# Kernel optimization log

Hardware: AMD Instinct MI355X
Metric: run time of the kernel (lower is better)

## Reference

```python
import jax, jax.numpy as jnp
import numpy as np

N = 50000          # nodes
E = 800000         # edges (avg degree 16)
C = 64             # hidden_channels
MC = 128           # message_channels = 2*C
EDGE_IN = 3 * C + 4
UPD_IN = C + MC + C


def _mlp(x, w1, b1, w2, b2, w3, b3):
    h1 = jax.nn.gelu(x @ w1 + b1, approximate=False)  # torch nn.GELU default = exact erf
    h2 = jax.nn.gelu(h1 @ w2 + b2, approximate=False)
    return h2 @ w3 + b3


def _layernorm(x, g, b, eps=1e-5):
    mu = x.mean(-1, keepdims=True)
    var = ((x - mu) ** 2).mean(-1, keepdims=True)
    return (x - mu) * jax.lax.rsqrt(var + eps) * g + b


def _forward(edge_index, coords, h, flow_dir, ln_g, ln_b,
             ew1, eb1, ew2, eb2, ew3, eb3,
             gw1, gb1, gw2, gb2,
             glw1, glb1, glw2, glb2, glw3, glb3,
             uw1, ub1, uw2, ub2, uw3, ub3, res_scale):
    x = coords[0]                       # [N,3]
    feat = _layernorm(h[0], ln_g, ln_b) # [N,C]
    u = flow_dir[0]
    u = u / (jnp.linalg.norm(u) + 1e-8)
    row, col = edge_index[0], edge_index[1]
    xi, xj = x[row], x[col]             # [E,3] gathers
    rel = xi - xj
    dist2 = (rel * rel).sum(-1, keepdims=True)
    xi_dot_u = (xi * u).sum(-1, keepdims=True)
    xj_dot_u = (xj * u).sum(-1, keepdims=True)
    rel_dot_u = (rel * u).sum(-1, keepdims=True)
    fi, fj = feat[row], feat[col]       # [E,C]
    fd = fi - fj
    edge_input = jnp.concatenate([fi, fj, fd, dist2, xi_dot_u, xj_dot_u, rel_dot_u], axis=-1)  # [E, 3C+4]
    edge_hidden = _mlp(edge_input, ew1, eb1, ew2, eb2, ew3, eb3)  # [E, MC]
    gate = jax.nn.sigmoid(jax.nn.gelu(edge_hidden @ gw1 + gb1, approximate=False) @ gw2 + gb2)  # [E,1]
    msg = gate * edge_hidden
    agg = jax.ops.segment_sum(msg, row, num_segments=N)                       # [N, MC]
    deg = jax.ops.segment_sum(jnp.ones((E, 1), feat.dtype), row, num_segments=N)
    agg = agg / jnp.maximum(deg, 1.0)
    global_feat = feat.mean(0, keepdims=True)                                  # [1,C]
    global_ctx = _mlp(global_feat, glw1, glb1, glw2, glb2, glw3, glb3)        # [1,C]
    global_node = jnp.broadcast_to(global_ctx, (feat.shape[0], global_ctx.shape[-1]))
    update_input = jnp.concatenate([feat, agg, global_node], axis=-1)          # [N, C+MC+C]
    dh = _mlp(update_input, uw1, ub1, uw2, ub2, uw3, ub3)                      # [N,C]
    return (jnp.tanh(res_scale) * dh)[None]                                    # [1,N,C]


def setup_inputs() -> dict:
    key = jax.random.key(0)
    ks = iter(jax.random.split(key, 40))
    def nrm(shape, scale=0.05):
        return (jax.random.normal(next(ks), shape, jnp.float32) * scale)
    return {
        "coords": jax.random.normal(next(ks), (1, N, 3), jnp.float32),
        "h": jax.random.normal(next(ks), (1, N, C), jnp.float32),
        "flow_dir": jax.random.normal(next(ks), (1, 3), jnp.float32),
        "edge_index": jax.random.randint(next(ks), (2, E), 0, N, dtype=jnp.int32),
        "ln_g": jnp.ones((C,), jnp.float32), "ln_b": jnp.zeros((C,), jnp.float32),
        "ew1": nrm((EDGE_IN, MC)), "eb1": jnp.zeros((MC,), jnp.float32),
        "ew2": nrm((MC, MC)), "eb2": jnp.zeros((MC,), jnp.float32),
        "ew3": nrm((MC, MC)), "eb3": jnp.zeros((MC,), jnp.float32),
        "gw1": nrm((MC, MC)), "gb1": jnp.zeros((MC,), jnp.float32),
        "gw2": nrm((MC, 1)), "gb2": jnp.zeros((1,), jnp.float32),
        "glw1": nrm((C, C)), "glb1": jnp.zeros((C,), jnp.float32),
        "glw2": nrm((C, C)), "glb2": jnp.zeros((C,), jnp.float32),
        "glw3": nrm((C, C)), "glb3": jnp.zeros((C,), jnp.float32),
        "uw1": nrm((UPD_IN, MC)), "ub1": jnp.zeros((MC,), jnp.float32),
        "uw2": nrm((MC, MC)), "ub2": jnp.zeros((MC,), jnp.float32),
        "uw3": nrm((MC, C)), "ub3": jnp.zeros((C,), jnp.float32),
        "res_scale": jnp.float32(0.15),
    }


def reference(coords, h, flow_dir, edge_index, ln_g, ln_b,
              ew1, eb1, ew2, eb2, ew3, eb3,
              gw1, gb1, gw2, gb2,
              glw1, glb1, glw2, glb2, glw3, glb3,
              uw1, ub1, uw2, ub2, uw3, ub3, res_scale):
    return _forward(edge_index, coords, h, flow_dir, ln_g, ln_b,
                    ew1, eb1, ew2, eb2, ew3, eb3,
                    gw1, gb1, gw2, gb2,
                    glw1, glb1, glw2, glb2, glw3, glb3,
                    uw1, ub1, uw2, ub2, uw3, ub3, res_scale)
```

## Files before the change

kernel.cpp:

```cpp
#include <hip/hip_runtime.h>
#include <hip/hip_bf16.h>
#include <math.h>

#define N_NODES 50000
#define N_EDGES 800000
#define CDIM 64
#define MCDIM 128
#define GSUM_REP 32

#define XS1 168
#define HS  136
#define UST 264

typedef __attribute__((ext_vector_type(8))) short short8;
typedef __attribute__((ext_vector_type(4))) float floatx4;
typedef __attribute__((ext_vector_type(2))) float f32x2;

__device__ __forceinline__ float gelu_fast(float x) {
    float z = fabsf(x) * 0.70710678f;
    float w = fmaf(z, fmaf(z, fmaf(z, fmaf(z, 0.078108f, 0.000972f),
                                   0.230389f), 0.278393f), 1.0f);
    float w2 = w * w;
    float r = __builtin_amdgcn_rcpf(w2 * w2);
    float m = 0.5f * fabsf(x);
    return fmaf(-m, r, fmaf(0.5f, x, m));
}

__device__ __forceinline__ f32x2 gelu_pk(f32x2 x) {
    f32x2 ax = __builtin_elementwise_abs(x);
    f32x2 z = ax * 0.70710678f;
    f32x2 w = z * (z * (z * (z * 0.078108f + 0.000972f) + 0.230389f)
                   + 0.278393f) + 1.0f;
    f32x2 w2 = w * w;
    f32x2 w4 = w2 * w2;
    f32x2 r;
    r.x = __builtin_amdgcn_rcpf(w4.x);
    r.y = __builtin_amdgcn_rcpf(w4.y);
    f32x2 m = 0.5f * ax;
    return 0.5f * x + m - m * r;
}

__device__ __forceinline__ unsigned short f2bf(float f) {
    unsigned int u = __float_as_uint(f);
    unsigned int r = u + 0x7fffu + ((u >> 16) & 1u);
    return (unsigned short)(r >> 16);
}
__device__ __forceinline__ float bf2f(unsigned int lo16) {
    return __uint_as_float(lo16 << 16);
}
__device__ __forceinline__ unsigned int f2bf2(float lo, float hi) {
    __hip_bfloat162 v = __float22bfloat162_rn(make_float2(lo, hi));
    union { __hip_bfloat162 b; unsigned int u; } cv;
    cv.b = v;
    return cv.u;
}
__device__ __forceinline__ ushort4 pack4(float4 v) {
    ushort4 r;
    r.x = f2bf(v.x); r.y = f2bf(v.y); r.z = f2bf(v.z); r.w = f2bf(v.w);
    return r;
}

#define F1_OFF 0
#define F2_OFF (5 * 4096)
#define F3_OFF (9 * 4096)
#define FG_OFF (13 * 4096)
#define FU1_OFF (17 * 4096)
#define FU2_OFF (25 * 4096)
#define FU3_OFF (29 * 4096)
#define FRAG_TOTAL (29 * 4096 + 4 * 2048)

__global__ __launch_bounds__(256) void prep_frags(
    const float* __restrict__ ew1, const float* __restrict__ ew2,
    const float* __restrict__ ew3, const float* __restrict__ gw1,
    const float* __restrict__ eb3, const float* __restrict__ gb1,
    const float* __restrict__ uw1, const float* __restrict__ uw2,
    const float* __restrict__ uw3, unsigned short* __restrict__ frags,
    int* __restrict__ deg_int, float* __restrict__ gsum,
    float* __restrict__ egb) {
    int idx = blockIdx.x * 256 + threadIdx.x;
    if (idx < N_NODES) deg_int[idx] = 0;
    if (idx < GSUM_REP * 64) gsum[idx] = 0.0f;
    if (idx < 128) {
        float s = gb1[idx];
        for (int jj = 0; jj < 128; jj++) s += eb3[jj] * gw1[jj * 128 + idx];
        egb[idx] = s;
    }
    if (idx >= FRAG_TOTAL) return;
    if (idx < F2_OFF) {
        int chunk = idx >> 12;
        int rem = idx & 4095;
        int ct = rem >> 9;
        int lane = (rem >> 3) & 63;
        int j = rem & 7;
        int k = chunk * 32 + (lane >> 4) * 8 + j;
        int n = ct * 16 + (lane & 15);
        float v;
        if (k < 64)       v = ew1[k * 128 + n] + ew1[(128 + k) * 128 + n];
        else if (k < 128) v = ew1[k * 128 + n] - ew1[(64 + k) * 128 + n];
        else if (k < 132) v = ew1[(192 + k - 128) * 128 + n];
        else              v = 0.0f;
        frags[idx] = f2bf(v);
    } else if (idx >= FG_OFF && idx < FU1_OFF) {
        int chunk = idx >> 12;
        int rem = idx & 4095;
        int ct = rem >> 9;
        int lane = (rem >> 3) & 63;
        int j = rem & 7;
        int k = (chunk - 13) * 32 + (lane >> 4) * 8 + j;
        int n = ct * 16 + (lane & 15);
        float s = 0.0f;
        for (int jj = 0; jj < 128; jj++) s += ew3[k * 128 + jj] * gw1[jj * 128 + n];
        frags[idx] = f2bf(s);
    } else if (idx < FU3_OFF) {
        int chunk = idx >> 12;
        int rem = idx & 4095;
        int ct = rem >> 9;
        int lane = (rem >> 3) & 63;
        int j = rem & 7;
        const float* W; int kbase;
        if (chunk < 9)       { W = ew2; kbase = (chunk - 5) * 32; }
        else if (chunk < 13) { W = ew3; kbase = (chunk - 9) * 32; }
        else if (chunk < 25) { W = uw1; kbase = (chunk - 17) * 32; }
        else                 { W = uw2; kbase = (chunk - 25) * 32; }
        int k = kbase + (lane >> 4) * 8 + j;
        int n = ct * 16 + (lane & 15);
        frags[idx] = f2bf(W[k * 128 + n]);
    } else {
        int rem = idx - FU3_OFF;
        int chunk = rem >> 11;
        int r = rem & 2047;
        int ct = r >> 9;
        int lane = (r >> 3) & 63;
        int j = r & 7;
        int k = chunk * 32 + (lane >> 4) * 8 + j;
        int n = ct * 16 + (lane & 15);
        frags[idx] = f2bf(uw3[k * 64 + n]);
    }
}

template <int NCT>
__device__ __forceinline__ void bias_init(floatx4* acc,
                                          const float* __restrict__ bias, int lane) {
    int c = lane & 15;
#pragma unroll
    for (int ct = 0; ct < NCT; ct++) {
        float b = bias[ct * 16 + c];
        acc[ct][0] = b; acc[ct][1] = b; acc[ct][2] = b; acc[ct][3] = b;
    }
}

template <int NCH, int NCT>
__device__ __forceinline__ void mfma_layer(const unsigned short* Xl, int xs,
                                           const unsigned short* __restrict__ F,
                                           int lane, floatx4* acc) {
    int q = lane >> 4, c = lane & 15;
    const unsigned short* xrow = Xl + c * xs + q * 8;
    for (int k0 = 0; k0 < NCH; k0++) {
        short8 a = *(const short8*)(xrow + k0 * 32);
#pragma unroll
        for (int ct = 0; ct < NCT; ct++) {
            short8 b = *(const short8*)(F + ((k0 * NCT + ct) * 64 + lane) * 8);
            acc[ct] = __builtin_amdgcn_mfma_f32_16x16x32_bf16(a, b, acc[ct], 0, 0, 0);
        }
    }
}

template <int NCH>
__device__ __forceinline__ void mfma_nsplit(const unsigned short* x1, int rstride,
                                            const unsigned short* __restrict__ F,
                                            int lane, int w2,
                                            floatx4 acc[4][2]) {
    int q = lane >> 4, c = lane & 15;
    for (int k0 = 0; k0 < NCH; k0++) {
        short8 b0 = *(const short8*)(F + (((k0 * 8 + w2) * 64) + lane) * 8);
        short8 b1 = *(const short8*)(F + (((k0 * 8 + w2 + 1) * 64) + lane) * 8);
#pragma unroll
        for (int rt = 0; rt < 4; rt++) {
            short8 a = *(const short8*)(x1 + rt * (16 * XS1) + c * rstride
                                        + q * 8 + k0 * 32);
            acc[rt][0] = __builtin_amdgcn_mfma_f32_16x16x32_bf16(a, b0, acc[rt][0], 0, 0, 0);
            acc[rt][1] = __builtin_amdgcn_mfma_f32_16x16x32_bf16(a, b1, acc[rt][1], 0, 0, 0);
        }
    }
}

__device__ __forceinline__ void bias_init2(floatx4 acc[4][2],
                                           const float* __restrict__ bias,
                                           int lane, int w) {
    int c = lane & 15;
    float b0 = bias[w * 32 + c], b1 = bias[w * 32 + 16 + c];
#pragma unroll
    for (int rt = 0; rt < 4; rt++) {
        acc[rt][0][0] = b0; acc[rt][0][1] = b0; acc[rt][0][2] = b0; acc[rt][0][3] = b0;
        acc[rt][1][0] = b1; acc[rt][1][1] = b1; acc[rt][1][2] = b1; acc[rt][1][3] = b1;
    }
}

__device__ __forceinline__ void epi2_store(floatx4 acc[4][2],
                                           unsigned short* x1, int lane, int w) {
    int q = lane >> 4, c = lane & 15;
#pragma unroll
    for (int rt = 0; rt < 4; rt++) {
        unsigned short* base = x1 + rt * (16 * XS1) + (q * 4) * HS + w * 32 + c;
#pragma unroll
        for (int ctl = 0; ctl < 2; ctl++) {
            f32x2 v01 = {acc[rt][ctl][0], acc[rt][ctl][1]};
            f32x2 v23 = {acc[rt][ctl][2], acc[rt][ctl][3]};
            v01 = gelu_pk(v01); v23 = gelu_pk(v23);
            unsigned int p01 = f2bf2(v01.x, v01.y), p23 = f2bf2(v23.x, v23.y);
            unsigned short* p = base + ctl * 16;
            p[0]      = (unsigned short)p01;
            p[HS]     = (unsigned short)(p01 >> 16);
            p[2 * HS] = (unsigned short)p23;
            p[3 * HS] = (unsigned short)(p23 >> 16);
        }
    }
}

template <bool GELU, int NCT>
__device__ __forceinline__ void epilogue_store(floatx4* acc,
                                               unsigned short* dst, int xs, int lane) {
    int q = lane >> 4, c = lane & 15;
    unsigned short* base = dst + (q * 4) * xs + c;
#pragma unroll
    for (int ct = 0; ct < NCT; ct++) {
        f32x2 v01 = {acc[ct][0], acc[ct][1]};
        f32x2 v23 = {acc[ct][2], acc[ct][3]};
        if (GELU) { v01 = gelu_pk(v01); v23 = gelu_pk(v23); }
        unsigned int p01 = f2bf2(v01.x, v01.y), p23 = f2bf2(v23.x, v23.y);
        unsigned short* p = base + ct * 16;
        p[0]      = (unsigned short)p01;
        p[xs]     = (unsigned short)(p01 >> 16);
        p[2 * xs] = (unsigned short)p23;
        p[3 * xs] = (unsigned short)(p23 >> 16);
    }
}

__global__ __launch_bounds__(256) void ln_count_kernel(
    const float* __restrict__ h, const float* __restrict__ ln_g,
    const float* __restrict__ ln_b, const float* __restrict__ flow_dir,
    const int* __restrict__ eidx, unsigned short* __restrict__ featb,
    float* __restrict__ gsum, float* __restrict__ u_out,
    int* __restrict__ deg_int) {
    int t = threadIdx.x;
    int ln = t >> 6;
    int c = t & 63;
    int n = blockIdx.x * 4 + ln;

    float x = h[n * CDIM + c];
    float s = x;
#pragma unroll
    for (int off = 32; off > 0; off >>= 1) s += __shfl_xor(s, off, 64);
    float mu = s * (1.0f / 64.0f);
    float d = x - mu;
    float v = d * d;
#pragma unroll
    for (int off = 32; off > 0; off >>= 1) v += __shfl_xor(v, off, 64);
    float rs = 1.0f / sqrtf(v * (1.0f / 64.0f) + 1e-5f);
    float f = d * rs * ln_g[c] + ln_b[c];
    featb[n * CDIM + c] = f2bf(f);

    __shared__ float fs[4][64];
    fs[ln][c] = f;
    __syncthreads();
    if (t < 64) {
        float p = fs[0][t] + fs[1][t] + fs[2][t] + fs[3][t];
        atomicAdd(&gsum[(blockIdx.x & (GSUM_REP - 1)) * 64 + t], p);
        int e = blockIdx.x * 64 + t;
        atomicAdd(&deg_int[eidx[e]], 1);
    }
    if (blockIdx.x == 0 && t == 0) {
        float ux = flow_dir[0], uy = flow_dir[1], uz = flow_dir[2];
        float nrm = sqrtf(ux * ux + uy * uy + uz * uz) + 1e-8f;
        u_out[0] = ux / nrm;
        u_out[1] = uy / nrm;
        u_out[2] = uz / nrm;
    }
}

__global__ __launch_bounds__(1024) void mid_kernel(
    const int* __restrict__ deg_int, int* __restrict__ rowstart,
    int* __restrict__ cursor,
    const float* __restrict__ gsum,
    const float* __restrict__ glw1, const float* __restrict__ glb1,
    const float* __restrict__ glw2, const float* __restrict__ glb2,
    const float* __restrict__ glw3, const float* __restrict__ glb3,
    const float* __restrict__ res_scale,
    unsigned short* __restrict__ gctxb, float* __restrict__ tres) {
    int t = threadIdx.x;
    if (blockIdx.x == 0) {
        __shared__ int wsum[16];
        __shared__ int run;
        int wid = t >> 6, lane = t & 63;
        int4 vs[13];
#pragma unroll
        for (int chunk = 0; chunk < 13; chunk++) {
            int base = chunk * 4096 + t * 4;
            int4 v = {0, 0, 0, 0};
            if (base + 3 < N_NODES) {
                v = *(const int4*)(deg_int + base);
            } else {
                if (base < N_NODES) v.x = deg_int[base];
                if (base + 1 < N_NODES) v.y = deg_int[base + 1];
                if (base + 2 < N_NODES) v.z = deg_int[base + 2];
                if (base + 3 < N_NODES) v.w = deg_int[base + 3];
            }
            vs[chunk] = v;
        }
        if (t == 0) run = 0;
        __syncthreads();
#pragma unroll
        for (int chunk = 0; chunk < 13; chunk++) {
            int base = chunk * 4096 + t * 4;
            int4 v = vs[chunk];
            int s1 = v.x, s2 = s1 + v.y, s3 = s2 + v.z, s4 = s3 + v.w;
            int x = s4;
#pragma unroll
            for (int off = 1; off < 64; off <<= 1) {
                int y = __shfl_up(x, off, 64);
                if (lane >= off) x += y;
            }
            if (lane == 63) wsum[wid] = x;
            __syncthreads();
            if (t < 16) {
                int sv = wsum[t];
#pragma unroll
                for (int off = 1; off < 16; off <<= 1) {
                    int y = __shfl_up(sv, off, 16);
                    if (t >= off) sv += y;
                }
                wsum[t] = sv;
            }
            __syncthreads();
            int run_l = run;
            int wpre = (wid == 0) ? 0 : wsum[wid - 1];
            int toff = run_l + wpre + (x - s4);
            int e0 = toff, e1 = toff + s1, e2 = toff + s2, e3 = toff + s3;
            if (base <= N_NODES) rowstart[base] = e0;
            if (base + 1 <= N_NODES) rowstart[base + 1] = e1;
            if (base + 2 <= N_NODES) rowstart[base + 2] = e2;
            if (base + 3 <= N_NODES) rowstart[base + 3] = e3;
            if (base < N_NODES) cursor[base] = e0;
            if (base + 1 < N_NODES) cursor[base + 1] = e1;
            if (base + 2 < N_NODES) cursor[base + 2] = e2;
            if (base + 3 < N_NODES) cursor[base + 3] = e3;
            __syncthreads();
            if (t == 0) run = run_l + wsum[15];
            __syncthreads();
        }
    } else {
        __shared__ float a[64], b[64];
        float s = 0.0f;
        if (t < 64) {
            float acc = 0.0f;
            for (int r = 0; r < GSUM_REP; r++) acc += gsum[r * 64 + t];
            a[t] = acc * (1.0f / (float)N_NODES);
        }
        __syncthreads();
        if (t < 64) {
            s = glb1[t];
            for (int k = 0; k < 64; k++) s += a[k] * glw1[k * 64 + t];
            b[t] = gelu_fast(s);
        }
        __syncthreads();
        if (t < 64) {
            s = glb2[t];
            for (int k = 0; k < 64; k++) s += b[k] * glw2[k * 64 + t];
        }
        __syncthreads();
        if (t < 64) a[t] = gelu_fast(s);
        __syncthreads();
        if (t < 64) {
            s = glb3[t];
            for (int k = 0; k < 64; k++) s += a[k] * glw3[k * 64 + t];
            gctxb[t] = f2bf(s);
        }
        if (t == 0) *tres = tanhf(res_scale[0]);
    }
}

struct SmemE {
    unsigned short x1[64 * XS1];
    float gatep[4][64];
    int pos[64];
    int rows[64];
};

__global__ __launch_bounds__(256, 6) void edge_kernel(
    const float* __restrict__ coords, const int* __restrict__ eidx,
    const unsigned short* __restrict__ featb, const float* __restrict__ u,
    const unsigned short* __restrict__ frags,
    const float* __restrict__ eb1, const float* __restrict__ eb2,
    const float* __restrict__ eb3,
    const float* __restrict__ egb, const float* __restrict__ gw2,
    const float* __restrict__ gb2,
    int* __restrict__ cursor, unsigned short* __restrict__ msg,
    float* __restrict__ agg, int use_msg) {
    __shared__ SmemE sm;
    int t = threadIdx.x;
    int wv = t >> 6;
    int lane = t & 63;
    int e0 = blockIdx.x * 64;
    int q = lane >> 4, c = lane & 15;
    int w2 = wv * 2;

    int rowreg;
    {
        int le = t >> 2, sub = t & 3;
        int e = e0 + le;
        int row = eidx[e];
        int col = eidx[N_EDGES + e];
        rowreg = row;
        const uint4* fi4 = (const uint4*)(featb + (long)row * CDIM);
        const uint4* fj4 = (const uint4*)(featb + (long)col * CDIM);
        unsigned short* xr = sm.x1 + le * XS1;
        *(uint4*)(xr + sub * 16) = fi4[sub * 2];
        *(uint4*)(xr + sub * 16 + 8) = fi4[sub * 2 + 1];
        *(uint4*)(xr + 64 + sub * 16) = fj4[sub * 2];
        *(uint4*)(xr + 64 + sub * 16 + 8) = fj4[sub * 2 + 1];
        ushort4 z = {0, 0, 0, 0};
        if (sub == 0) {
            sm.rows[le] = row;
            float xix = coords[row * 3], xiy = coords[row * 3 + 1], xiz = coords[row * 3 + 2];
            float xjx = coords[col * 3], xjy = coords[col * 3 + 1], xjz = coords[col * 3 + 2];
            float rx = xix - xjx, ry = xiy - xjy, rz = xiz - xjz;
            float ux = u[0], uy = u[1], uz = u[2];
            float4 sc;
            sc.x = rx * rx + ry * ry + rz * rz;
            sc.y = xix * ux + xiy * uy + xiz * uz;
            sc.z = xjx * ux + xjy * uy + xjz * uz;
            sc.w = rx * ux + ry * uy + rz * uz;
            *(ushort4*)(xr + 128) = pack4(sc);
        } else if (sub == 1) {
            *(ushort4*)(xr + 132) = z; *(ushort4*)(xr + 136) = z; *(ushort4*)(xr + 140) = z;
        } else if (sub == 2) {
            *(ushort4*)(xr + 144) = z; *(ushort4*)(xr + 148) = z;
        } else {
            *(ushort4*)(xr + 152) = z; *(ushort4*)(xr + 156) = z;
        }
    }
    __syncthreads();

    floatx4 acc[4][2];

    bias_init2(acc, eb1, lane, wv);
    mfma_nsplit<5>(sm.x1, XS1, frags + F1_OFF, lane, w2, acc);
    __syncthreads();
    epi2_store(acc, sm.x1, lane, wv);
    __syncthreads();

    bias_init2(acc, eb2, lane, wv);
    mfma_nsplit<4>(sm.x1, HS, frags + F2_OFF, lane, w2, acc);
    __syncthreads();
    epi2_store(acc, sm.x1, lane, wv);
    __syncthreads();

    int posreg = 0;
    if (use_msg && (t & 3) == 0) posreg = atomicAdd(&cursor[rowreg], 1);

    bias_init2(acc, egb, lane, wv);
    mfma_nsplit<4>(sm.x1, HS, frags + FG_OFF, lane, w2, acc);
    {
#pragma unroll
        for (int rt = 0; rt < 4; rt++) {
            float w2v0 = gw2[wv * 32 + c];
            float w2v1 = gw2[wv * 32 + 16 + c];
            f32x2 g01a = gelu_pk((f32x2){acc[rt][0][0], acc[rt][0][1]});
            f32x2 g23a = gelu_pk((f32x2){acc[rt][0][2], acc[rt][0][3]});
            f32x2 g01b = gelu_pk((f32x2){acc[rt][1][0], acc[rt][1][1]});
            f32x2 g23b = gelu_pk((f32x2){acc[rt][1][2], acc[rt][1][3]});
            float p[4];
            p[0] = g01a.x * w2v0 + g01b.x * w2v1;
            p[1] = g01a.y * w2v0 + g01b.y * w2v1;
            p[2] = g23a.x * w2v0 + g23b.x * w2v1;
            p[3] = g23a.y * w2v0 + g23b.y * w2v1;
#pragma unroll
            for (int i = 0; i < 4; i++) {
#pragma unroll
                for (int mask = 1; mask < 16; mask <<= 1)
                    p[i] += __shfl_xor(p[i], mask, 64);
            }
            if (c == 0) {
#pragma unroll
                for (int i = 0; i < 4; i++)
                    sm.gatep[wv][rt * 16 + q * 4 + i] = p[i];
            }
        }
    }

    floatx4 acch[4][2];
    bias_init2(acch, eb3, lane, wv);
    mfma_nsplit<4>(sm.x1, HS, frags + F3_OFF, lane, w2, acch);
    __syncthreads();

    float gb = gb2[0];
    float g4[4][4];
#pragma unroll
    for (int rt = 0; rt < 4; rt++) {
#pragma unroll
        for (int i = 0; i < 4; i++) {
            int e = rt * 16 + q * 4 + i;
            float z = sm.gatep[0][e] + sm.gatep[1][e] + sm.gatep[2][e]
                    + sm.gatep[3][e] + gb;
            g4[rt][i] = 1.0f / (1.0f + __expf(-z));
        }
    }

    if (use_msg) {
        {
#pragma unroll
            for (int rt = 0; rt < 4; rt++) {
                unsigned short* base = sm.x1 + rt * (16 * XS1) + (q * 4) * HS
                                     + wv * 32 + c;
#pragma unroll
                for (int ctl = 0; ctl < 2; ctl++) {
                    unsigned int p01 = f2bf2(acch[rt][ctl][0] * g4[rt][0],
                                             acch[rt][ctl][1] * g4[rt][1]);
                    unsigned int p23 = f2bf2(acch[rt][ctl][2] * g4[rt][2],
                                             acch[rt][ctl][3] * g4[rt][3]);
                    unsigned short* p = base + ctl * 16;
                    p[0]      = (unsigned short)p01;
                    p[HS]     = (unsigned short)(p01 >> 16);
                    p[2 * HS] = (unsigned short)p23;
                    p[3 * HS] = (unsigned short)(p23 >> 16);
                }
            }
        }
        if ((t & 3) == 0) sm.pos[t >> 2] = posreg;
        __syncthreads();
        {
            int le = t >> 2, sub = t & 3;
            long base = (long)sm.pos[le] * MCDIM;
            const unsigned short* src = sm.x1 + (le >> 4) * 16 * XS1 + (le & 15) * HS;
#pragma unroll
            for (int m = 0; m < 4; m++) {
                int off = m * 32 + sub * 8;
                *(short8*)(msg + base + off) = *(const short8*)(src + off);
            }
        }
    } else {
#pragma unroll
        for (int rt = 0; rt < 4; rt++) {
#pragma unroll
            for (int i = 0; i < 4; i++) {
                int row = sm.rows[rt * 16 + q * 4 + i];
                float* agr = agg + (long)row * MCDIM + wv * 32 + c;
#pragma unroll
                for (int ctl = 0; ctl < 2; ctl++)
                    atomicAdd(agr + ctl * 16, g4[rt][i] * acch[rt][ctl][i]);
            }
        }
    }
}

__global__ __launch_bounds__(256) void gather_kernel(
    const int* __restrict__ rowstart, const unsigned short* __restrict__ msg,
    const float* __restrict__ agg, int use_msg,
    unsigned short* __restrict__ aggb) {
    int wv = threadIdx.x >> 6, lane = threadIdx.x & 63;
    int n = blockIdx.x * 4 + wv;
    if (n >= N_NODES) return;
    int rs = rowstart[n], re = rowstart[n + 1];
    int deg = re - rs;
    float a0 = 0.0f, a1 = 0.0f, a2 = 0.0f, a3 = 0.0f;
    if (use_msg) {
        const unsigned short* base = msg + (long)rs * MCDIM;
        int pairs = deg >> 1;
        for (int i = 0; i < pairs; i++) {
            uint2 v = *(const uint2*)(base + i * 256 + lane * 4);
            a0 += bf2f(v.x & 0xffffu); a1 += bf2f(v.x >> 16);
            a2 += bf2f(v.y & 0xffffu); a3 += bf2f(v.y >> 16);
        }
        if ((deg & 1) && lane < 32) {
            uint2 v = *(const uint2*)(base + (deg - 1) * MCDIM + lane * 4);
            a0 += bf2f(v.x & 0xffffu); a1 += bf2f(v.x >> 16);
            a2 += bf2f(v.y & 0xffffu); a3 += bf2f(v.y >> 16);
        }
        a0 += __shfl_xor(a0, 32, 64);
        a1 += __shfl_xor(a1, 32, 64);
        a2 += __shfl_xor(a2, 32, 64);
        a3 += __shfl_xor(a3, 32, 64);
    } else if (lane < 32) {
        const float4 v = *(const float4*)(agg + (long)n * MCDIM + lane * 4);
        a0 = v.x; a1 = v.y; a2 = v.z; a3 = v.w;
    }
    if (lane < 32) {
        float inv = 1.0f / fmaxf((float)deg, 1.0f);
        uint2 o;
        o.x = f2bf2(a0 * inv, a1 * inv);
        o.y = f2bf2(a2 * inv, a3 * inv);
        *(uint2*)(aggb + (long)n * MCDIM + lane * 4) = o;
    }
}

struct SmemU {
    unsigned short ui[64 * UST];
};

__global__ __launch_bounds__(256, 4) void update_kernel(
    const unsigned short* __restrict__ featb, const unsigned short* __restrict__ aggb,
    const unsigned short* __restrict__ gctxb, const float* __restrict__ tres,
    const unsigned short* __restrict__ frags,
    const float* __restrict__ ub1, const float* __restrict__ ub2,
    const float* __restrict__ ub3,
    float* __restrict__ out) {
    __shared__ SmemU sm;
    int t = threadIdx.x;
    int wv = t >> 6;
    int lane = t & 63;
    int n0 = blockIdx.x * 64;
    unsigned short* slice = sm.ui + wv * 16 * UST;

    {
        int ln = t >> 2, sub = t & 3;
        int n = n0 + ln;
        unsigned short* ur = sm.ui + ln * UST;
        if (n < N_NODES) {
            const uint4* f4 = (const uint4*)(featb + (long)n * CDIM);
            *(uint4*)(ur + sub * 16) = f4[sub * 2];
            *(uint4*)(ur + sub * 16 + 8) = f4[sub * 2 + 1];
            const uint4* a4 = (const uint4*)(aggb + (long)n * MCDIM);
            *(uint4*)(ur + 64 + sub * 32) = a4[sub * 4];
            *(uint4*)(ur + 64 + sub * 32 + 8) = a4[sub * 4 + 1];
            *(uint4*)(ur + 64 + sub * 32 + 16) = a4[sub * 4 + 2];
            *(uint4*)(ur + 64 + sub * 32 + 24) = a4[sub * 4 + 3];
            const uint4* g4 = (const uint4*)gctxb;
            *(uint4*)(ur + 192 + sub * 16) = g4[sub * 2];
            *(uint4*)(ur + 192 + sub * 16 + 8) = g4[sub * 2 + 1];
        } else {
            uint4 z = {0, 0, 0, 0};
#pragma unroll
            for (int m = 0; m < 8; m++) *(uint4*)(ur + sub * 64 + m * 8) = z;
        }
    }
    __syncthreads();

    floatx4 acc[8];
    bias_init<8>(acc, ub1, lane);
    mfma_layer<8, 8>(slice, UST, frags + FU1_OFF, lane, acc);
    epilogue_store<true, 8>(acc, slice, HS, lane);
    __syncthreads();

    bias_init<8>(acc, ub2, lane);
    mfma_layer<4, 8>(slice, HS, frags + FU2_OFF, lane, acc);
    epilogue_store<true, 8>(acc, slice, HS, lane);
    __syncthreads();

    floatx4 acc3[4];
    bias_init<4>(acc3, ub3, lane);
    mfma_layer<4, 4>(slice, HS, frags + FU3_OFF, lane, acc3);
    {
        int q = lane >> 4, c = lane & 15;
        float tr = *tres;
#pragma unroll
        for (int ct = 0; ct < 4; ct++) {
#pragma unroll
            for (int i = 0; i < 4; i++) {
                int n = n0 + wv * 16 + q * 4 + i;
                if (n < N_NODES) out[(long)n * CDIM + ct * 16 + c] = acc3[ct][i] * tr;
            }
        }
    }
}

extern "C" void kernel_launch(void* const* d_in, const int* in_sizes, int n_in,
                              void* d_out, int out_size, void* d_ws, size_t ws_size,
                              hipStream_t stream) {
    const float* coords = (const float*)d_in[0];
    const float* h = (const float*)d_in[1];
    const float* flow = (const float*)d_in[2];
    const int* eidx = (const int*)d_in[3];
    const float* ln_g = (const float*)d_in[4];
    const float* ln_b = (const float*)d_in[5];
    const float* ew1 = (const float*)d_in[6];
    const float* eb1 = (const float*)d_in[7];
    const float* ew2 = (const float*)d_in[8];
    const float* eb2 = (const float*)d_in[9];
    const float* ew3 = (const float*)d_in[10];
    const float* eb3 = (const float*)d_in[11];
    const float* gw1 = (const float*)d_in[12];
    const float* gb1 = (const float*)d_in[13];
    const float* gw2 = (const float*)d_in[14];
    const float* gb2 = (const float*)d_in[15];
    const float* glw1 = (const float*)d_in[16];
    const float* glb1 = (const float*)d_in[17];
    const float* glw2 = (const float*)d_in[18];
    const float* glb2 = (const float*)d_in[19];
    const float* glw3 = (const float*)d_in[20];
    const float* glb3 = (const float*)d_in[21];
    const float* uw1 = (const float*)d_in[22];
    const float* ub1 = (const float*)d_in[23];
    const float* uw2 = (const float*)d_in[24];
    const float* ub2 = (const float*)d_in[25];
    const float* uw3 = (const float*)d_in[26];
    const float* ub3 = (const float*)d_in[27];
    const float* res = (const float*)d_in[28];

    char* base = (char*)d_ws;
    unsigned short* frags = (unsigned short*)base;
    unsigned short* featb = (unsigned short*)(base + FRAG_TOTAL * 2);
    unsigned short* aggb = featb + (size_t)N_NODES * CDIM;
    unsigned short* gctxb = aggb + (size_t)N_NODES * MCDIM;
    float* gsum = (float*)(gctxb + 64);
    float* u = gsum + GSUM_REP * 64;
    float* tres = u + 4;
    float* egb = tres + 1;
    int* rowstart = (int*)(egb + 128);
    int* cursor = rowstart + (N_NODES + 1);
    int* deg_int = cursor + N_NODES;
    char* tail = (char*)(deg_int + N_NODES);
    tail = (char*)(((uintptr_t)tail + 255) & ~(uintptr_t)255);
    size_t head_bytes = (size_t)(tail - base);
    size_t msg_bytes = (size_t)N_EDGES * MCDIM * 2;
    int use_msg = (ws_size >= head_bytes + msg_bytes) ? 1 : 0;
    unsigned short* msg = (unsigned short*)tail;
    float* agg = (float*)tail;

    if (!use_msg)
        hipMemsetAsync(agg, 0, (size_t)N_NODES * MCDIM * sizeof(float), stream);

    prep_frags<<<FRAG_TOTAL / 256, 256, 0, stream>>>(ew1, ew2, ew3, gw1,
                                                     eb3, gb1,
                                                     uw1, uw2, uw3, frags,
                                                     deg_int, gsum, egb);
    ln_count_kernel<<<N_NODES / 4, 256, 0, stream>>>(h, ln_g, ln_b, flow, eidx,
                                                     featb, gsum, u, deg_int);
    mid_kernel<<<2, 1024, 0, stream>>>(deg_int, rowstart, cursor, gsum,
                                       glw1, glb1, glw2, glb2, glw3, glb3,
                                       res, gctxb, tres);
    edge_kernel<<<N_EDGES / 64, 256, 0, stream>>>(coords, eidx, featb, u, frags,
                                                  eb1, eb2, eb3, egb, gw2, gb2,
                                                  cursor, msg, agg, use_msg);
    gather_kernel<<<(N_NODES + 3) / 4, 256, 0, stream>>>(rowstart, msg, agg,
                                                         use_msg, aggb);
    update_kernel<<<(N_NODES + 63) / 64, 256, 0, stream>>>(featb, aggb, gctxb,
                                                           tres, frags,
                                                           ub1, ub2, ub3,
                                                           (float*)d_out);
}
```

Baseline: 455.9 us.

## Fuse CSR message gather into update kernel and raise edge kernel occupancy

When the message buffer path is active, the update kernel now reduces each node's CSR-sorted bf16 messages itself and writes the mean aggregate straight into shared memory. This removes the separate gather kernel launch and the round trip of the aggregated bf16 tensor through global memory. The edge kernel's launch bound also rises from 6 to 7 blocks per CU, which may force register spilling. The fused gather runs serially per wave over 16 nodes, so load imbalance and latency exposure inside the update kernel could offset the saved traffic.

```diff
diff --git a/kernel.cpp b/kernel.cpp
--- a/kernel.cpp
+++ b/kernel.cpp
@@ -386,7 +386,7 @@
     int rows[64];
 };
 
-__global__ __launch_bounds__(256, 6) void edge_kernel(
+__global__ __launch_bounds__(256, 7) void edge_kernel(
     const float* __restrict__ coords, const int* __restrict__ eidx,
     const unsigned short* __restrict__ featb, const float* __restrict__ u,
     const unsigned short* __restrict__ frags,
@@ -599,11 +599,12 @@
 
 __global__ __launch_bounds__(256, 4) void update_kernel(
     const unsigned short* __restrict__ featb, const unsigned short* __restrict__ aggb,
+    const int* __restrict__ rowstart, const unsigned short* __restrict__ msg,
     const unsigned short* __restrict__ gctxb, const float* __restrict__ tres,
     const unsigned short* __restrict__ frags,
     const float* __restrict__ ub1, const float* __restrict__ ub2,
     const float* __restrict__ ub3,
-    float* __restrict__ out) {
+    float* __restrict__ out, int use_msg) {
     __shared__ SmemU sm;
     int t = threadIdx.x;
     int wv = t >> 6;
@@ -619,11 +620,13 @@
             const uint4* f4 = (const uint4*)(featb + (long)n * CDIM);
             *(uint4*)(ur + sub * 16) = f4[sub * 2];
             *(uint4*)(ur + sub * 16 + 8) = f4[sub * 2 + 1];
-            const uint4* a4 = (const uint4*)(aggb + (long)n * MCDIM);
-            *(uint4*)(ur + 64 + sub * 32) = a4[sub * 4];
-            *(uint4*)(ur + 64 + sub * 32 + 8) = a4[sub * 4 + 1];
-            *(uint4*)(ur + 64 + sub * 32 + 16) = a4[sub * 4 + 2];
-            *(uint4*)(ur + 64 + sub * 32 + 24) = a4[sub * 4 + 3];
+            if (!use_msg) {
+                const uint4* a4 = (const uint4*)(aggb + (long)n * MCDIM);
+                *(uint4*)(ur + 64 + sub * 32) = a4[sub * 4];
+                *(uint4*)(ur + 64 + sub * 32 + 8) = a4[sub * 4 + 1];
+                *(uint4*)(ur + 64 + sub * 32 + 16) = a4[sub * 4 + 2];
+                *(uint4*)(ur + 64 + sub * 32 + 24) = a4[sub * 4 + 3];
+            }
             const uint4* g4 = (const uint4*)gctxb;
             *(uint4*)(ur + 192 + sub * 16) = g4[sub * 2];
             *(uint4*)(ur + 192 + sub * 16 + 8) = g4[sub * 2 + 1];
@@ -631,6 +634,39 @@
             uint4 z = {0, 0, 0, 0};
 #pragma unroll
             for (int m = 0; m < 8; m++) *(uint4*)(ur + sub * 64 + m * 8) = z;
+        }
+    }
+
+    if (use_msg) {
+        for (int ln2 = 0; ln2 < 16; ln2++) {
+            int n = n0 + wv * 16 + ln2;
+            if (n >= N_NODES) break;
+            int rs = rowstart[n], re = rowstart[n + 1];
+            int deg = re - rs;
+            float a0 = 0.0f, a1 = 0.0f, a2 = 0.0f, a3 = 0.0f;
+            const unsigned short* basep = msg + (long)rs * MCDIM;
+            int pairs = deg >> 1;
+            for (int i = 0; i < pairs; i++) {
+                uint2 v = *(const uint2*)(basep + i * 256 + lane * 4);
+                a0 += bf2f(v.x & 0xffffu); a1 += bf2f(v.x >> 16);
+                a2 += bf2f(v.y & 0xffffu); a3 += bf2f(v.y >> 16);
+            }
+            if ((deg & 1) && lane < 32) {
+                uint2 v = *(const uint2*)(basep + (deg - 1) * MCDIM + lane * 4);
+                a0 += bf2f(v.x & 0xffffu); a1 += bf2f(v.x >> 16);
+                a2 += bf2f(v.y & 0xffffu); a3 += bf2f(v.y >> 16);
+            }
+            a0 += __shfl_xor(a0, 32, 64);
+            a1 += __shfl_xor(a1, 32, 64);
+            a2 += __shfl_xor(a2, 32, 64);
+            a3 += __shfl_xor(a3, 32, 64);
+            if (lane < 32) {
+                float inv = 1.0f / fmaxf((float)deg, 1.0f);
+                uint2 o;
+                o.x = f2bf2(a0 * inv, a1 * inv);
+                o.y = f2bf2(a2 * inv, a3 * inv);
+                *(uint2*)(sm.ui + (wv * 16 + ln2) * UST + 64 + lane * 4) = o;
+            }
         }
     }
     __syncthreads();
@@ -731,10 +767,12 @@
     edge_kernel<<<N_EDGES / 64, 256, 0, stream>>>(coords, eidx, featb, u, frags,
                                                   eb1, eb2, eb3, egb, gw2, gb2,
                                                   cursor, msg, agg, use_msg);
-    gather_kernel<<<(N_NODES + 3) / 4, 256, 0, stream>>>(rowstart, msg, agg,
-                                                         use_msg, aggb);
-    update_kernel<<<(N_NODES + 63) / 64, 256, 0, stream>>>(featb, aggb, gctxb,
-                                                           tres, frags,
+    if (!use_msg)
+        gather_kernel<<<(N_NODES + 3) / 4, 256, 0, stream>>>(rowstart, msg, agg,
+                                                             use_msg, aggb);
+    update_kernel<<<(N_NODES + 63) / 64, 256, 0, stream>>>(featb, aggb,
+                                                           rowstart, msg,
+                                                           gctxb, tres, frags,
                                                            ub1, ub2, ub3,
-                                                           (float*)d_out);
-}
+                                                           (float*)d_out, use_msg);
+}
```

Measured after the change: 481.3 us. 5.6% more time.

## Split update MLP across output columns per wave and unroll message gather

Applied to the files above, without the earlier changes.

The update kernel switches from each wave owning 16 rows and all output columns to each wave owning all 64 rows and a slice of output columns, the same N-split scheme the edge kernel uses. This lets each weight fragment loaded from global memory be reused across four row tiles, cutting weight traffic per block, but it adds barriers between the MMA and epilogue phases because outputs now overwrite rows other waves still read. Separately, the CSR aggregation loop is unrolled by two with independent accumulators to expose more memory-level parallelism.

```diff
diff --git a/kernel.cpp b/kernel.cpp
--- a/kernel.cpp
+++ b/kernel.cpp
@@ -166,7 +166,8 @@
 }
 
 template <int NCH>
-__device__ __forceinline__ void mfma_nsplit(const unsigned short* x1, int rstride,
+__device__ __forceinline__ void mfma_nsplit(const unsigned short* x1,
+                                            int tilestride, int rstride,
                                             const unsigned short* __restrict__ F,
                                             int lane, int w2,
                                             floatx4 acc[4][2]) {
@@ -176,7 +177,7 @@
         short8 b1 = *(const short8*)(F + (((k0 * 8 + w2 + 1) * 64) + lane) * 8);
 #pragma unroll
         for (int rt = 0; rt < 4; rt++) {
-            short8 a = *(const short8*)(x1 + rt * (16 * XS1) + c * rstride
+            short8 a = *(const short8*)(x1 + rt * tilestride + c * rstride
                                         + q * 8 + k0 * 32);
             acc[rt][0] = __builtin_amdgcn_mfma_f32_16x16x32_bf16(a, b0, acc[rt][0], 0, 0, 0);
             acc[rt][1] = __builtin_amdgcn_mfma_f32_16x16x32_bf16(a, b1, acc[rt][1], 0, 0, 0);
@@ -197,11 +198,12 @@
 }
 
 __device__ __forceinline__ void epi2_store(floatx4 acc[4][2],
-                                           unsigned short* x1, int lane, int w) {
+                                           unsigned short* x1, int tilestride,
+                                           int lane, int w) {
     int q = lane >> 4, c = lane & 15;
 #pragma unroll
     for (int rt = 0; rt < 4; rt++) {
-        unsigned short* base = x1 + rt * (16 * XS1) + (q * 4) * HS + w * 32 + c;
+        unsigned short* base = x1 + rt * tilestride + (q * 4) * HS + w * 32 + c;
 #pragma unroll
         for (int ctl = 0; ctl < 2; ctl++) {
             f32x2 v01 = {acc[rt][ctl][0], acc[rt][ctl][1]};
@@ -214,25 +216,6 @@
             p[2 * HS] = (unsigned short)p23;
             p[3 * HS] = (unsigned short)(p23 >> 16);
         }
-    }
-}
-
-template <bool GELU, int NCT>
-__device__ __forceinline__ void epilogue_store(floatx4* acc,
-                                               unsigned short* dst, int xs, int lane) {
-    int q = lane >> 4, c = lane & 15;
-    unsigned short* base = dst + (q * 4) * xs + c;
-#pragma unroll
-    for (int ct = 0; ct < NCT; ct++) {
-        f32x2 v01 = {acc[ct][0], acc[ct][1]};
-        f32x2 v23 = {acc[ct][2], acc[ct][3]};
-        if (GELU) { v01 = gelu_pk(v01); v23 = gelu_pk(v23); }
-        unsigned int p01 = f2bf2(v01.x, v01.y), p23 = f2bf2(v23.x, v23.y);
-        unsigned short* p = base + ct * 16;
-        p[0]      = (unsigned short)p01;
-        p[xs]     = (unsigned short)(p01 >> 16);
-        p[2 * xs] = (unsigned short)p23;
-        p[3 * xs] = (unsigned short)(p23 >> 16);
     }
 }
 
@@ -444,22 +427,22 @@
     floatx4 acc[4][2];
 
     bias_init2(acc, eb1, lane, wv);
-    mfma_nsplit<5>(sm.x1, XS1, frags + F1_OFF, lane, w2, acc);
-    __syncthreads();
-    epi2_store(acc, sm.x1, lane, wv);
+    mfma_nsplit<5>(sm.x1, 16 * XS1, XS1, frags + F1_OFF, lane, w2, acc);
+    __syncthreads();
+    epi2_store(acc, sm.x1, 16 * XS1, lane, wv);
     __syncthreads();
 
     bias_init2(acc, eb2, lane, wv);
-    mfma_nsplit<4>(sm.x1, HS, frags + F2_OFF, lane, w2, acc);
-    __syncthreads();
-    epi2_store(acc, sm.x1, lane, wv);
+    mfma_nsplit<4>(sm.x1, 16 * XS1, HS, frags + F2_OFF, lane, w2, acc);
+    __syncthreads();
+    epi2_store(acc, sm.x1, 16 * XS1, lane, wv);
     __syncthreads();
 
     int posreg = 0;
     if (use_msg && (t & 3) == 0) posreg = atomicAdd(&cursor[rowreg], 1);
 
     bias_init2(acc, egb, lane, wv);
-    mfma_nsplit<4>(sm.x1, HS, frags + FG_OFF, lane, w2, acc);
+    mfma_nsplit<4>(sm.x1, 16 * XS1, HS, frags + FG_OFF, lane, w2, acc);
     {
 #pragma unroll
         for (int rt = 0; rt < 4; rt++) {
@@ -490,7 +473,7 @@
 
     floatx4 acch[4][2];
     bias_init2(acch, eb3, lane, wv);
-    mfma_nsplit<4>(sm.x1, HS, frags + F3_OFF, lane, w2, acch);
+    mfma_nsplit<4>(sm.x1, 16 * XS1, HS, frags + F3_OFF, lane, w2, acch);
     __syncthreads();
 
     float gb = gb2[0];
@@ -566,11 +549,22 @@
     if (use_msg) {
         const unsigned short* base = msg + (long)rs * MCDIM;
         int pairs = deg >> 1;
-        for (int i = 0; i < pairs; i++) {
+        float b0 = 0.0f, b1 = 0.0f, b2 = 0.0f, b3 = 0.0f;
+        int i = 0;
+        for (; i + 1 < pairs; i += 2) {
+            uint2 v = *(const uint2*)(base + i * 256 + lane * 4);
+            uint2 w = *(const uint2*)(base + (i + 1) * 256 + lane * 4);
+            a0 += bf2f(v.x & 0xffffu); a1 += bf2f(v.x >> 16);
+            a2 += bf2f(v.y & 0xffffu); a3 += bf2f(v.y >> 16);
+            b0 += bf2f(w.x & 0xffffu); b1 += bf2f(w.x >> 16);
+            b2 += bf2f(w.y & 0xffffu); b3 += bf2f(w.y >> 16);
+        }
+        if (i < pairs) {
             uint2 v = *(const uint2*)(base + i * 256 + lane * 4);
             a0 += bf2f(v.x & 0xffffu); a1 += bf2f(v.x >> 16);
             a2 += bf2f(v.y & 0xffffu); a3 += bf2f(v.y >> 16);
         }
+        a0 += b0; a1 += b1; a2 += b2; a3 += b3;
         if ((deg & 1) && lane < 32) {
             uint2 v = *(const uint2*)(base + (deg - 1) * MCDIM + lane * 4);
             a0 += bf2f(v.x & 0xffffu); a1 += bf2f(v.x >> 16);
@@ -609,7 +603,8 @@
     int wv = t >> 6;
     int lane = t & 63;
     int n0 = blockIdx.x * 64;
-    unsigned short* slice = sm.ui + wv * 16 * UST;
+    int q = lane >> 4, c = lane & 15;
+    int w2 = wv * 2;
 
     {
         int ln = t >> 2, sub = t & 3;
@@ -635,29 +630,47 @@
     }
     __syncthreads();
 
-    floatx4 acc[8];
-    bias_init<8>(acc, ub1, lane);
-    mfma_layer<8, 8>(slice, UST, frags + FU1_OFF, lane, acc);
-    epilogue_store<true, 8>(acc, slice, HS, lane);
-    __syncthreads();
-
-    bias_init<8>(acc, ub2, lane);
-    mfma_layer<4, 8>(slice, HS, frags + FU2_OFF, lane, acc);
-    epilogue_store<true, 8>(acc, slice, HS, lane);
+    floatx4 acc[4][2];
+
+    bias_init2(acc, ub1, lane, wv);
+    mfma_nsplit<8>(sm.ui, 16 * UST, UST, frags + FU1_OFF, lane, w2, acc);
+    __syncthreads();
+    epi2_store(acc, sm.ui, 16 * UST, lane, wv);
+    __syncthreads();
+
+    bias_init2(acc, ub2, lane, wv);
+    mfma_nsplit<4>(sm.ui, 16 * UST, HS, frags + FU2_OFF, lane, w2, acc);
+    __syncthreads();
+    epi2_store(acc, sm.ui, 16 * UST, lane, wv);
     __syncthreads();
 
     floatx4 acc3[4];
-    bias_init<4>(acc3, ub3, lane);
-    mfma_layer<4, 4>(slice, HS, frags + FU3_OFF, lane, acc3);
     {
-        int q = lane >> 4, c = lane & 15;
+        float b = ub3[wv * 16 + c];
+#pragma unroll
+        for (int rt = 0; rt < 4; rt++) {
+            acc3[rt][0] = b; acc3[rt][1] = b; acc3[rt][2] = b; acc3[rt][3] = b;
+        }
+        for (int k0 = 0; k0 < 4; k0++) {
+            short8 bf = *(const short8*)(frags + FU3_OFF + k0 * 2048
+                                         + wv * 512 + lane * 8);
+#pragma unroll
+            for (int rt = 0; rt < 4; rt++) {
+                short8 a = *(const short8*)(sm.ui + rt * (16 * UST) + c * HS
+                                            + q * 8 + k0 * 32);
+                acc3[rt] = __builtin_amdgcn_mfma_f32_16x16x32_bf16(a, bf, acc3[rt], 0, 0, 0);
+            }
+        }
+    }
+    {
         float tr = *tres;
 #pragma unroll
-        for (int ct = 0; ct < 4; ct++) {
+        for (int rt = 0; rt < 4; rt++) {
 #pragma unroll
             for (int i = 0; i < 4; i++) {
-                int n = n0 + wv * 16 + q * 4 + i;
-                if (n < N_NODES) out[(long)n * CDIM + ct * 16 + c] = acc3[ct][i] * tr;
+                int n = n0 + rt * 16 + q * 4 + i;
+                if (n < N_NODES)
+                    out[(long)n * CDIM + wv * 16 + c] = acc3[rt][i] * tr;
             }
         }
     }
```

Result: no change. 462.6 us (+1.5%).
